# Performance work log

Measured on AMD Instinct MI355X. Metric: run time of the kernel, lower is better.

The kernel has to match this reference:

```python
import jax, jax.numpy as jnp
import numpy as np

EPS = 1e-5


def _layer(x, g, b, W_in, b_in, W_h, b_h, W_out, b_out):
    # x: [B, T, D]
    mu = jnp.mean(x, axis=-1, keepdims=True)
    var = jnp.mean(jnp.square(x - mu), axis=-1, keepdims=True)
    x_n = (x - mu) * jax.lax.rsqrt(var + EPS) * g + b
    # in_proj for all timesteps at once (same math as per-step linear)
    uv = jnp.einsum('btd,ed->bte', x_n, W_in) + b_in  # [B, T, 2D]
    d = x.shape[-1]
    u = jnp.transpose(uv[..., :d], (1, 0, 2))  # [T, B, D]
    v = jnp.transpose(uv[..., d:], (1, 0, 2))  # [T, B, D]

    def step(h, uv_t):
        u_t, v_t = uv_t
        gate = jax.nn.sigmoid(u_t)
        cand = jnp.tanh(v_t + h @ W_h.T + b_h)
        h_new = gate * cand + (1.0 - gate) * h
        y = h_new @ W_out.T + b_out
        return h_new, y

    h0 = jnp.zeros((x.shape[0], d), dtype=x.dtype)
    _, ys = jax.lax.scan(step, h0, (u, v))  # ys: [T, B, D]
    return x + jnp.transpose(ys, (1, 0, 2))


def setup_inputs() -> dict:
    key = jax.random.key(0)
    B, T, D, L = 8, 2048, 1024, 2
    ks = jax.random.split(key, 8)
    s = 1.0 / np.sqrt(D)
    return {
        'x': jax.random.normal(ks[0], (B, T, D), dtype=jnp.float32),
        'ln_g': jnp.ones((L, D), dtype=jnp.float32),
        'ln_b': jnp.zeros((L, D), dtype=jnp.float32),
        'W_in': jax.random.normal(ks[1], (L, 2 * D, D), dtype=jnp.float32) * s,
        'b_in': jnp.zeros((L, 2 * D), dtype=jnp.float32),
        'W_h': jax.random.normal(ks[2], (L, D, D), dtype=jnp.float32) * s,
        'b_h': jnp.zeros((L, D), dtype=jnp.float32),
        'W_out': jax.random.normal(ks[3], (L, D, D), dtype=jnp.float32) * s,
        'b_out': jnp.zeros((L, D), dtype=jnp.float32),
    }


def reference(x, ln_g, ln_b, W_in, b_in, W_h, b_h, W_out, b_out):
    out = x
    for l in range(W_in.shape[0]):  # small fixed n_layers loop
        out = _layer(out, ln_g[l], ln_b[l], W_in[l], b_in[l], W_h[l], b_h[l],
                     W_out[l], b_out[l])
    return out
```

## Files before the change

### kernel.cpp

```cpp
#include <hip/hip_runtime.h>
#include <stdint.h>
#include <stddef.h>

typedef __bf16 bf16;
typedef __bf16 bf16x8 __attribute__((ext_vector_type(8)));
typedef __bf16 bf16x4 __attribute__((ext_vector_type(4)));
typedef float  f32x4  __attribute__((ext_vector_type(4)));

#define B_ 8
#define T_ 2048
#define D_ 1024
#define L_ 2

#define AS1C(p) ((const __attribute__((address_space(1))) void*)(p))
#define AS3(p)  ((__attribute__((address_space(3))) void*)(p))


__global__ __launch_bounds__(256) void cvt_kernel(const float* __restrict__ in,
                                                  bf16* __restrict__ out, int n4) {
  int i = blockIdx.x * 256 + threadIdx.x;
  if (i >= n4) return;
  float4 v = ((const float4*)in)[i];
  bf16x4 o = { (bf16)v.x, (bf16)v.y, (bf16)v.z, (bf16)v.w };
  ((bf16x4*)out)[i] = o;
}

__global__ __launch_bounds__(256) void ln_kernel(const float* __restrict__ x,
                                                 const float* __restrict__ g,
                                                 const float* __restrict__ b,
                                                 bf16* __restrict__ xn) {
  const int row = blockIdx.x;
  const int tid = threadIdx.x;
  const float4 v = ((const float4*)(x + (size_t)row * D_))[tid];
  float s1 = v.x + v.y + v.z + v.w;
  float s2 = v.x * v.x + v.y * v.y + v.z * v.z + v.w * v.w;
#pragma unroll
  for (int off = 1; off < 64; off <<= 1) {
    s1 += __shfl_xor(s1, off);
    s2 += __shfl_xor(s2, off);
  }
  __shared__ float r1[4], r2[4];
  if ((tid & 63) == 0) { r1[tid >> 6] = s1; r2[tid >> 6] = s2; }
  __syncthreads();
  s1 = r1[0] + r1[1] + r1[2] + r1[3];
  s2 = r2[0] + r2[1] + r2[2] + r2[3];
  const float mu = s1 * (1.f / D_);
  const float var = s2 * (1.f / D_) - mu * mu;
  const float rs = rsqrtf(var + 1e-5f);
  const float4 gv = ((const float4*)g)[tid];
  const float4 bv = ((const float4*)b)[tid];
  bf16x4 o = { (bf16)((v.x - mu) * rs * gv.x + bv.x),
               (bf16)((v.y - mu) * rs * gv.y + bv.y),
               (bf16)((v.z - mu) * rs * gv.z + bv.z),
               (bf16)((v.w - mu) * rs * gv.w + bv.w) };
  ((bf16x4*)(xn + (size_t)row * D_))[tid] = o;
}

__global__ __launch_bounds__(256) void prep2_kernel(const float* __restrict__ Win2,
    const float* __restrict__ g2, const float* __restrict__ be2,
    const float* __restrict__ bin2, bf16* __restrict__ W2p,
    float* __restrict__ csum, float* __restrict__ cbias) {
  const int n = blockIdx.x;
  const int tid = threadIdx.x;
  const float4 w4 = ((const float4*)(Win2 + (size_t)n * 1024))[tid];
  const float4 g4 = ((const float4*)g2)[tid];
  const float4 b4 = ((const float4*)be2)[tid];
  bf16x4 o = { (bf16)(g4.x * w4.x), (bf16)(g4.y * w4.y),
               (bf16)(g4.z * w4.z), (bf16)(g4.w * w4.w) };
  ((bf16x4*)(W2p + (size_t)n * 1024))[tid] = o;
  float s = (float)o[0] + (float)o[1] + (float)o[2] + (float)o[3];
  float cbv = b4.x * w4.x + b4.y * w4.y + b4.z * w4.z + b4.w * w4.w;
#pragma unroll
  for (int off = 1; off < 64; off <<= 1) {
    s += __shfl_xor(s, off);
    cbv += __shfl_xor(cbv, off);
  }
  __shared__ float rs_[4], rc_[4];
  if ((tid & 63) == 0) { rs_[tid >> 6] = s; rc_[tid >> 6] = cbv; }
  __syncthreads();
  if (tid == 0) {
    csum[n] = rs_[0] + rs_[1] + rs_[2] + rs_[3];
    cbias[n] = rc_[0] + rc_[1] + rc_[2] + rc_[3] + bin2[n];
  }
}

__global__ __launch_bounds__(256) void gemm_uv(const bf16* __restrict__ A,
                                               const bf16* __restrict__ Bw,
                                               const float* __restrict__ bias,
                                               bf16* __restrict__ uvp,
                                               int M, int N, int K) {
  __shared__ bf16 As[128 * 32];
  __shared__ bf16 Bs[128 * 32];
  const int tid = threadIdx.x;
  const int lane = tid & 63;
  const int wave = tid >> 6;
  const int m0 = blockIdx.y * 128;
  const int n0 = blockIdx.x * 128;
  const int wm = (wave >> 1) * 64;
  const int wn = (wave & 1) * 64;
  f32x4 acc[4][4] = {};

  for (int kt = 0; kt < K; kt += 32) {
#pragma unroll
    for (int it = 0; it < 2; ++it) {
      const int gidx = it * 256 + tid;
      const int row = gidx >> 2;
      const int col = (gidx & 3) << 3;
      __builtin_amdgcn_global_load_lds(AS1C(A + (size_t)(m0 + row) * K + kt + col),
                                       AS3(&As[gidx * 8]), 16, 0, 0);
      __builtin_amdgcn_global_load_lds(AS1C(Bw + (size_t)(n0 + row) * K + kt + col),
                                       AS3(&Bs[gidx * 8]), 16, 0, 0);
    }
    __syncthreads();
    bf16x8 af[4], bfr[4];
#pragma unroll
    for (int i = 0; i < 4; ++i)
      af[i] = *(const bf16x8*)&As[(wm + i * 16 + (lane & 15)) * 32 + (lane >> 4) * 8];
#pragma unroll
    for (int j = 0; j < 4; ++j)
      bfr[j] = *(const bf16x8*)&Bs[(wn + j * 16 + (lane & 15)) * 32 + (lane >> 4) * 8];
#pragma unroll
    for (int i = 0; i < 4; ++i)
#pragma unroll
      for (int j = 0; j < 4; ++j)
        acc[i][j] = __builtin_amdgcn_mfma_f32_16x16x32_bf16(af[i], bfr[j], acc[i][j], 0, 0, 0);
    __syncthreads();
  }

  const int cr = (lane >> 4) * 4;
  const int cc = lane & 15;
#pragma unroll
  for (int i = 0; i < 4; ++i) {
#pragma unroll
    for (int j = 0; j < 4; ++j) {
      const int mb = m0 + wm + i * 16 + cr;
      const int n = n0 + wn + j * 16 + cc;
      const float bn = bias[n];
      const int p = n >> 10;
      const int nn2 = n & 1023;
#pragma unroll
      for (int r = 0; r < 4; ++r) {
        const int row = mb + r;
        const int b = row >> 11;
        const int t = row & (T_ - 1);
        uvp[(size_t)p * T_ * 8192 + (size_t)t * 8192 + nn2 * 8 + b] =
            (bf16)(acc[i][j][r] + bn);
      }
    }
  }
}

__global__ __launch_bounds__(256) void gemm_hfrag(const char* __restrict__ Hb,
                                                  const bf16* __restrict__ Bw,
                                                  const float* __restrict__ bias,
                                                  const char* __restrict__ residF,
                                                  float* __restrict__ C,
                                                  int M, int N, int K) {
  __shared__ bf16 As[128 * 32];
  __shared__ bf16 Bs[128 * 32];
  const int tid = threadIdx.x;
  const int lane = tid & 63;
  const int wave = tid >> 6;
  const int m0 = blockIdx.y * 128;
  const int n0 = blockIdx.x * 128;
  const int wm = (wave >> 1) * 64;
  const int wn = (wave & 1) * 64;
  f32x4 acc[4][4] = {};

  for (int kt = 0; kt < K; kt += 32) {
#pragma unroll
    for (int it = 0; it < 2; ++it) {
      const int g = it * 256 + tid;
      const int r = g >> 2;
      const int sub = g & 3;
      const int R = m0 + r;
      const int bb = R >> 11;
      const int tt = R & (T_ - 1);
      const char* src = Hb + (size_t)tt * 16384 + (size_t)(kt >> 5) * 512
                        + (sub * 8 + bb) * 16;
      __builtin_amdgcn_global_load_lds(AS1C(src), AS3(&As[g * 8]), 16, 0, 0);
      __builtin_amdgcn_global_load_lds(AS1C(Bw + (size_t)(n0 + r) * K + kt + (sub << 3)),
                                       AS3(&Bs[g * 8]), 16, 0, 0);
    }
    __syncthreads();
    bf16x8 af[4], bfr[4];
#pragma unroll
    for (int i = 0; i < 4; ++i)
      af[i] = *(const bf16x8*)&As[(wm + i * 16 + (lane & 15)) * 32 + (lane >> 4) * 8];
#pragma unroll
    for (int j = 0; j < 4; ++j)
      bfr[j] = *(const bf16x8*)&Bs[(wn + j * 16 + (lane & 15)) * 32 + (lane >> 4) * 8];
#pragma unroll
    for (int i = 0; i < 4; ++i)
#pragma unroll
      for (int j = 0; j < 4; ++j)
        acc[i][j] = __builtin_amdgcn_mfma_f32_16x16x32_bf16(af[i], bfr[j], acc[i][j], 0, 0, 0);
    __syncthreads();
  }

  const int cr = (lane >> 4) * 4;
  const int cc = lane & 15;
#pragma unroll
  for (int i = 0; i < 4; ++i) {
#pragma unroll
    for (int j = 0; j < 4; ++j) {
      const int mb = m0 + wm + i * 16 + cr;
      const int n = n0 + wn + j * 16 + cc;
      const float bn = bias[n];
      const int foffn = (n >> 5) * 512 + (((n & 31) >> 3) * 8) * 16 + (n & 7) * 2;
#pragma unroll
      for (int r = 0; r < 4; ++r) {
        const int row = mb + r;
        const int b = row >> 11;
        const int tt2 = row & (T_ - 1);
        const float resid =
            (float)*(const bf16*)(residF + (size_t)tt2 * 16384 + foffn + b * 16);
        C[(size_t)row * N + n] = acc[i][j][r] + bn + resid;
      }
    }
  }
}

__device__ __forceinline__ void load_wb(bf16x8 (&wB)[32], const bf16* Wrow) {
  const int half = ((threadIdx.x & 63) >> 4) << 3;
#pragma unroll
  for (int kk = 0; kk < 32; ++kk)
    wB[kk] = *(const bf16x8*)(Wrow + kk * 32 + half);
#pragma unroll
  for (int kk = 0; kk < 32; ++kk)
    asm volatile("" : "+a"(wB[kk]));
}

__device__ __forceinline__ f32x4 frag_matvec(const char* __restrict__ dF, int rdoff,
                                             const bf16x8 (&wB)[32]) {
  f32x4 a0 = {0.f, 0.f, 0.f, 0.f}, a1 = a0, a2 = a0, a3 = a0;
#pragma unroll
  for (int kk = 0; kk < 32; kk += 4) {
    bf16x8 f0 = *(const bf16x8*)(dF + kk * 512 + rdoff);
    bf16x8 f1 = *(const bf16x8*)(dF + (kk + 1) * 512 + rdoff);
    bf16x8 f2 = *(const bf16x8*)(dF + (kk + 2) * 512 + rdoff);
    bf16x8 f3 = *(const bf16x8*)(dF + (kk + 3) * 512 + rdoff);
    a0 = __builtin_amdgcn_mfma_f32_16x16x32_bf16(f0, wB[kk], a0, 0, 0, 0);
    a1 = __builtin_amdgcn_mfma_f32_16x16x32_bf16(f1, wB[kk + 1], a1, 0, 0, 0);
    a2 = __builtin_amdgcn_mfma_f32_16x16x32_bf16(f2, wB[kk + 2], a2, 0, 0, 0);
    a3 = __builtin_amdgcn_mfma_f32_16x16x32_bf16(f3, wB[kk + 3], a3, 0, 0, 0);
  }
  return (a0 + a1) + (a2 + a3);
}

__device__ __forceinline__ void poll8(const unsigned* base, unsigned tgt) {
  const int lane = threadIdx.x & 63;
  unsigned sv = tgt;
  if (lane < 8)
    sv = __hip_atomic_load(base + lane * 16, __ATOMIC_RELAXED, __HIP_MEMORY_SCOPE_AGENT);
  while (!__all((int)(sv >= tgt))) {
    __builtin_amdgcn_s_sleep(1);
    if (lane < 8)
      sv = __hip_atomic_load(base + lane * 16, __ATOMIC_RELAXED, __HIP_MEMORY_SCOPE_AGENT);
  }
  (void)__hip_atomic_load(base, __ATOMIC_ACQUIRE, __HIP_MEMORY_SCOPE_AGENT);
}

__device__ __forceinline__ void poll2s3(const unsigned* sync, int wg, unsigned tgt) {
  const int lane = threadIdx.x & 63;
  unsigned sv = tgt;
  if (lane < 2)
    sv = __hip_atomic_load(sync + 256 + ((lane ? 8 : 0) + wg) * 16,
                           __ATOMIC_RELAXED, __HIP_MEMORY_SCOPE_AGENT);
  while (!__all((int)(sv >= tgt))) {
    __builtin_amdgcn_s_sleep(1);
    if (lane < 2)
      sv = __hip_atomic_load(sync + 256 + ((lane ? 8 : 0) + wg) * 16,
                             __ATOMIC_RELAXED, __HIP_MEMORY_SCOPE_AGENT);
  }
  (void)__hip_atomic_load(sync + 256, __ATOMIC_ACQUIRE, __HIP_MEMORY_SCOPE_AGENT);
}

template <bool GATED>
__device__ __forceinline__ void scan_gang(int wg, const bf16* uvU, const bf16* uvV,
    const bf16* Wh, const float* bh, char* Hb, unsigned* sync, int ownBase,
    char (*hC)[16384], char (*tscr)[256]) {
  const int tid = threadIdx.x;
  const int lane = tid & 63;
  const int wv = tid >> 6;
  const int Wg = wg * 8 + wv;
  const int n0 = Wg * 16;
  const int c = lane & 15;

  bf16x8 wB[32];
  load_wb(wB, Wh + ((size_t)(n0 + c) << 10));

  const float bh_n = bh[n0 + c];
  const int b0 = (lane >> 4) * 4;
  const int rdoff = ((lane >> 4) * 8 + (lane & 7)) * 16;
  const int wregion = Wg * 256;

  float hs0 = 0.f, hs1 = 0.f, hs2 = 0.f, hs3 = 0.f;

  bf16x4 uq = {}, vq = {};
  if (GATED) poll2s3(sync, wg, 1u);
  if (lane < 32) {
    uq = *(const bf16x4*)(uvU + (n0 + c) * 8 + b0);
    vq = *(const bf16x4*)(uvV + (n0 + c) * 8 + b0);
  }

  for (int t = 0; t < T_; ++t) {
    f32x4 asum = {0.f, 0.f, 0.f, 0.f};
    if (t > 0) {
      poll8(sync + ownBase, (unsigned)t);
      __builtin_amdgcn_sched_barrier(0);
      const char* srcF = Hb + (size_t)(t - 1) * 16384;
      char* dstF = hC[t & 1];
      __builtin_amdgcn_global_load_lds(AS1C(srcF + tid * 16), AS3(dstF + tid * 16), 16, 0, 0);
      __builtin_amdgcn_global_load_lds(AS1C(srcF + (512 + tid) * 16),
                                       AS3(dstF + (512 + tid) * 16), 16, 0, 0);
      __syncthreads();
      asum = frag_matvec(dstF, rdoff, wB);
    }

    char* wscr = tscr[wv];
    if (lane < 32) {
#pragma unroll
      for (int r = 0; r < 4; ++r) {
        const float uu = (float)uq[r];
        const float vv = (float)vq[r];
        float& hh = (r == 0) ? hs0 : (r == 1) ? hs1 : (r == 2) ? hs2 : hs3;
        const float s = asum[r] + bh_n + vv;
        const float gg = __builtin_amdgcn_rcpf(1.f + __expf(-uu));
        const float e = __expf(2.f * s);
        const float cand = 1.f - 2.f * __builtin_amdgcn_rcpf(e + 1.f);
        hh = fmaf(gg, cand - hh, hh);
        *(bf16*)(wscr + (c >> 3) * 128 + (b0 + r) * 16 + (c & 7) * 2) = (bf16)hh;
      }
    }
    asm volatile("s_waitcnt lgkmcnt(0)" ::: "memory");
    __builtin_amdgcn_sched_barrier(0);
    if (lane < 32) {
      const unsigned long long pv = *(const unsigned long long*)(wscr + lane * 8);
      char* dst = Hb + (size_t)t * 16384 + wregion + lane * 8;
      __hip_atomic_store((unsigned long long*)dst, pv,
                         __ATOMIC_RELAXED, __HIP_MEMORY_SCOPE_AGENT);
    }
    __syncthreads();
    if (tid == 0)
      __hip_atomic_store(sync + ownBase + wg * 16, (unsigned)(t + 1),
                         __ATOMIC_RELEASE, __HIP_MEMORY_SCOPE_AGENT);
    __builtin_amdgcn_sched_barrier(0);
    if (t < T_ - 1) {
      if (GATED) poll2s3(sync, wg, (unsigned)(t + 2));
      if (lane < 32) {
        uq = *(const bf16x4*)(uvU + (size_t)(t + 1) * 8192 + (n0 + c) * 8 + b0);
        vq = *(const bf16x4*)(uvV + (size_t)(t + 1) * 8192 + (n0 + c) * 8 + b0);
      }
    }
  }
}

__device__ __forceinline__ void s2_gang(int wg, const char* H1, const bf16* Wout,
    const float* bout, const float* x, char* out1F, unsigned* sync,
    char (*hC)[16384], char (*tscr)[256]) {
  const int tid = threadIdx.x;
  const int lane = tid & 63;
  const int wv = tid >> 6;
  const int W2 = wg * 8 + wv;
  const int n0 = W2 * 16;
  const int c = lane & 15;

  bf16x8 wB[32];
  load_wb(wB, Wout + ((size_t)(n0 + c) << 10));

  const float bo = bout[n0 + c];
  const int b0 = (lane >> 4) * 4;
  const int rdoff = ((lane >> 4) * 8 + (lane & 7)) * 16;
  const int wregion = W2 * 256;

  f32x4 xq = {0.f, 0.f, 0.f, 0.f};
  if (lane < 32) {
#pragma unroll
    for (int r = 0; r < 4; ++r)
      xq[r] = x[((size_t)(b0 + r) * T_) * 1024 + n0 + c];
  }

  for (int t = 0; t < T_; ++t) {
    poll8(sync, (unsigned)(t + 1));
    __builtin_amdgcn_sched_barrier(0);
    const char* srcF = H1 + (size_t)t * 16384;
    char* dstF = hC[t & 1];
    __builtin_amdgcn_global_load_lds(AS1C(srcF + tid * 16), AS3(dstF + tid * 16), 16, 0, 0);
    __builtin_amdgcn_global_load_lds(AS1C(srcF + (512 + tid) * 16),
                                     AS3(dstF + (512 + tid) * 16), 16, 0, 0);
    __syncthreads();
    f32x4 asum = frag_matvec(dstF, rdoff, wB);

    char* wscr = tscr[wv];
    if (lane < 32) {
#pragma unroll
      for (int r = 0; r < 4; ++r) {
        const float o = xq[r] + asum[r] + bo;
        *(bf16*)(wscr + (c >> 3) * 128 + (b0 + r) * 16 + (c & 7) * 2) = (bf16)o;
      }
    }
    asm volatile("s_waitcnt lgkmcnt(0)" ::: "memory");
    __builtin_amdgcn_sched_barrier(0);
    if (lane < 32) {
      const unsigned long long pv = *(const unsigned long long*)(wscr + lane * 8);
      char* dst = out1F + (size_t)t * 16384 + wregion + lane * 8;
      __hip_atomic_store((unsigned long long*)dst, pv,
                         __ATOMIC_RELAXED, __HIP_MEMORY_SCOPE_AGENT);
    }
    __syncthreads();
    if (tid == 0)
      __hip_atomic_store(sync + 128 + wg * 16, (unsigned)(t + 1),
                         __ATOMIC_RELEASE, __HIP_MEMORY_SCOPE_AGENT);
    __builtin_amdgcn_sched_barrier(0);
    if (t < T_ - 1 && lane < 32) {
#pragma unroll
      for (int r = 0; r < 4; ++r)
        xq[r] = x[((size_t)(b0 + r) * T_ + (t + 1)) * 1024 + n0 + c];
    }
  }
}

__device__ __forceinline__ void s3_gang(int wg, const char* out1F, const bf16* W2p,
    const float* csum2, const float* cbias2, bf16* uv2, unsigned* sync,
    char (*hC)[16384], char (*tscr)[256], float* smu, float* srs) {
  const int tid = threadIdx.x;
  const int lane = tid & 63;
  const int wv = tid >> 6;
  const int W3 = wg * 8 + wv;
  const int c = lane & 15;
  const int n = W3 * 16 + c;

  bf16x8 wB[32];
  load_wb(wB, W2p + ((size_t)n << 10));

  const float cs = csum2[n];
  const float cb = cbias2[n];
  const int b0 = (lane >> 4) * 4;
  const int rdoff = ((lane >> 4) * 8 + (lane & 7)) * 16;
  char* outPlane = (char*)(uv2 + (size_t)(W3 >> 6) * T_ * 8192);
  const int nn = (W3 & 63) * 16;

  for (int t = 0; t < T_; ++t) {
    poll8(sync + 128, (unsigned)(t + 1));
    __builtin_amdgcn_sched_barrier(0);
    const char* srcF = out1F + (size_t)t * 16384;
    char* dstF = hC[t & 1];
    __builtin_amdgcn_global_load_lds(AS1C(srcF + tid * 16), AS3(dstF + tid * 16), 16, 0, 0);
    __builtin_amdgcn_global_load_lds(AS1C(srcF + (512 + tid) * 16),
                                     AS3(dstF + (512 + tid) * 16), 16, 0, 0);
    __syncthreads();
    {
      float s1 = 0.f, s2 = 0.f;
#pragma unroll
      for (int gi = 0; gi < 2; ++gi) {
        const int gr = lane * 2 + gi;
        bf16x8 v8 = *(const bf16x8*)(dstF + (gr >> 2) * 512 + ((gr & 3) * 8 + wv) * 16);
#pragma unroll
        for (int j = 0; j < 8; ++j) {
          const float f = (float)v8[j];
          s1 += f;
          s2 += f * f;
        }
      }
#pragma unroll
      for (int off = 1; off < 64; off <<= 1) {
        s1 += __shfl_xor(s1, off);
        s2 += __shfl_xor(s2, off);
      }
      if (lane == 0) {
        const float mu = s1 * (1.f / 1024.f);
        const float var = s2 * (1.f / 1024.f) - mu * mu;
        smu[wv] = mu;
        srs[wv] = rsqrtf(var + 1e-5f);
      }
    }
    __syncthreads();
    f32x4 asum = frag_matvec(dstF, rdoff, wB);

    char* wscr = tscr[wv];
    if (lane < 32) {
#pragma unroll
      for (int r = 0; r < 4; ++r) {
        const int b = b0 + r;
        const float val = srs[b] * (asum[r] - smu[b] * cs) + cb;
        *(bf16*)(wscr + c * 16 + b * 2) = (bf16)val;
      }
    }
    asm volatile("s_waitcnt lgkmcnt(0)" ::: "memory");
    __builtin_amdgcn_sched_barrier(0);
    if (lane < 32) {
      const unsigned long long pv = *(const unsigned long long*)(wscr + lane * 8);
      char* dst = outPlane + (size_t)t * 16384 + nn * 16 + lane * 8;
      __hip_atomic_store((unsigned long long*)dst, pv,
                         __ATOMIC_RELAXED, __HIP_MEMORY_SCOPE_AGENT);
    }
    __syncthreads();
    if (tid == 0)
      __hip_atomic_store(sync + 256 + wg * 16, (unsigned)(t + 1),
                         __ATOMIC_RELEASE, __HIP_MEMORY_SCOPE_AGENT);
    __builtin_amdgcn_sched_barrier(0);
  }
}

__global__ __launch_bounds__(512, 1) void mega_kernel(
    const bf16* __restrict__ uv1, const bf16* __restrict__ Wh,
    const float* __restrict__ bh, const bf16* __restrict__ Wout,
    const float* __restrict__ bout, const float* __restrict__ x,
    const bf16* __restrict__ W2p, const float* __restrict__ csum2,
    const float* __restrict__ cbias2, char* __restrict__ H1,
    char* __restrict__ out1F, bf16* __restrict__ uv2, char* __restrict__ H2,
    unsigned* __restrict__ sync) {
  __shared__ __align__(16) char hC[2][16384];
  __shared__ __align__(16) char tscr[8][256];
  __shared__ float smu[8], srs[8];
  const int bid = blockIdx.x;
  if (bid < 8) {
    scan_gang<false>(bid, uv1, uv1 + (size_t)T_ * 8192, Wh, bh, H1, sync, 0, hC, tscr);
  } else if (bid < 16) {
    s2_gang(bid - 8, H1, Wout, bout, x, out1F, sync, hC, tscr);
  } else if (bid < 32) {
    s3_gang(bid - 16, out1F, W2p, csum2, cbias2, uv2, sync, hC, tscr, smu, srs);
  } else {
    scan_gang<true>(bid - 32, uv2, uv2 + (size_t)T_ * 8192,
                    Wh + (size_t)D_ * D_, bh + D_, H2, sync, 512, hC, tscr);
  }
}

extern "C" void kernel_launch(void* const* d_in, const int* in_sizes, int n_in,
                              void* d_out, int out_size, void* d_ws, size_t ws_size,
                              hipStream_t stream) {
  const float* x     = (const float*)d_in[0];
  const float* ln_g  = (const float*)d_in[1];
  const float* ln_b  = (const float*)d_in[2];
  const float* W_in  = (const float*)d_in[3];
  const float* b_in  = (const float*)d_in[4];
  const float* W_h   = (const float*)d_in[5];
  const float* b_h   = (const float*)d_in[6];
  const float* W_out = (const float*)d_in[7];
  const float* b_out = (const float*)d_in[8];
  float* out = (float*)d_out;

  char* ws = (char*)d_ws;
  size_t off = 0;
  auto alloc = [&](size_t bytes) -> void* {
    void* p = ws + off;
    off = (off + bytes + 255) & ~(size_t)255;
    return p;
  };
  bf16* wInB   = (bf16*)alloc((size_t)L_ * 2 * D_ * D_ * 2);
  bf16* wHB    = (bf16*)alloc((size_t)L_ * D_ * D_ * 2);
  bf16* wOutB  = (bf16*)alloc((size_t)L_ * D_ * D_ * 2);
  bf16* W2p    = (bf16*)alloc((size_t)2 * D_ * D_ * 2);
  float* csum2 = (float*)alloc(2 * D_ * 4);
  float* cbias2= (float*)alloc(2 * D_ * 4);
  bf16* Xn     = (bf16*)alloc((size_t)B_ * T_ * D_ * 2);
  char* H2     = (char*)Xn;
  bf16* uvp1   = (bf16*)alloc((size_t)2 * T_ * 8192 * 2);
  char* H1     = (char*)alloc((size_t)T_ * 16384);
  char* out1F  = (char*)alloc((size_t)T_ * 16384);
  bf16* uvp2   = (bf16*)alloc((size_t)2 * T_ * 8192 * 2);
  unsigned* sync = (unsigned*)alloc(4096);
  (void)ws_size; (void)in_sizes; (void)n_in; (void)out_size;

  {
    int n4 = L_ * 2 * D_ * D_ / 4;
    cvt_kernel<<<(n4 + 255) / 256, 256, 0, stream>>>(W_in, wInB, n4);
    n4 = L_ * D_ * D_ / 4;
    cvt_kernel<<<(n4 + 255) / 256, 256, 0, stream>>>(W_h, wHB, n4);
    cvt_kernel<<<(n4 + 255) / 256, 256, 0, stream>>>(W_out, wOutB, n4);
  }
  prep2_kernel<<<2 * D_, 256, 0, stream>>>(W_in + (size_t)2 * D_ * D_,
                                           ln_g + D_, ln_b + D_, b_in + 2 * D_,
                                           W2p, csum2, cbias2);

  const int Mrows = B_ * T_;
  ln_kernel<<<Mrows, 256, 0, stream>>>(x, ln_g, ln_b, Xn);

  dim3 g1(2 * D_ / 128, Mrows / 128);
  gemm_uv<<<g1, 256, 0, stream>>>(Xn, wInB, b_in, uvp1, Mrows, 2 * D_, D_);

  hipMemsetAsync(sync, 0, 4096, stream);
  mega_kernel<<<40, 512, 0, stream>>>(uvp1, wHB, b_h, wOutB, b_out, x,
                                      W2p, csum2, cbias2, H1, out1F, uvp2, H2, sync);

  dim3 g2(D_ / 128, Mrows / 128);
  gemm_hfrag<<<g2, 256, 0, stream>>>(H2, wOutB + (size_t)D_ * D_, b_out + D_,
                                     out1F, out, Mrows, D_, D_);
}
```

Baseline: 11.37 ms.

## Prefetch next timestep into LDS and merge LayerNorm stats into one barrier

The s2 and s3 gangs now poll for step t+1 and issue its async global-to-LDS copy at the end of step t, so the copy overlaps the loop tail and the next barrier rather than sitting on the critical path. In s3, per-row partial sums are written to shared memory and combined after the matvec, which removes the separate barrier that came before the matvec. The scan gangs still depend on these stages each step, so the gain may be small. The double-buffered LDS reuse relies on the barrier ordering being correct.

```diff
diff --git a/kernel.cpp b/kernel.cpp
--- a/kernel.cpp
+++ b/kernel.cpp
@@ -276,6 +276,12 @@
   (void)__hip_atomic_load(sync + 256, __ATOMIC_ACQUIRE, __HIP_MEMORY_SCOPE_AGENT);
 }
 
+__device__ __forceinline__ void stage16k(const char* srcF, char* dstF, int tid) {
+  __builtin_amdgcn_global_load_lds(AS1C(srcF + tid * 16), AS3(dstF + tid * 16), 16, 0, 0);
+  __builtin_amdgcn_global_load_lds(AS1C(srcF + (512 + tid) * 16),
+                                   AS3(dstF + (512 + tid) * 16), 16, 0, 0);
+}
+
 template <bool GATED>
 __device__ __forceinline__ void scan_gang(int wg, const bf16* uvU, const bf16* uvV,
     const bf16* Wh, const float* bh, char* Hb, unsigned* sync, int ownBase,
@@ -309,13 +315,9 @@
     if (t > 0) {
       poll8(sync + ownBase, (unsigned)t);
       __builtin_amdgcn_sched_barrier(0);
-      const char* srcF = Hb + (size_t)(t - 1) * 16384;
-      char* dstF = hC[t & 1];
-      __builtin_amdgcn_global_load_lds(AS1C(srcF + tid * 16), AS3(dstF + tid * 16), 16, 0, 0);
-      __builtin_amdgcn_global_load_lds(AS1C(srcF + (512 + tid) * 16),
-                                       AS3(dstF + (512 + tid) * 16), 16, 0, 0);
+      stage16k(Hb + (size_t)(t - 1) * 16384, hC[t & 1], tid);
       __syncthreads();
-      asum = frag_matvec(dstF, rdoff, wB);
+      asum = frag_matvec(hC[t & 1], rdoff, wB);
     }
 
     char* wscr = tscr[wv];
@@ -381,16 +383,13 @@
       xq[r] = x[((size_t)(b0 + r) * T_) * 1024 + n0 + c];
   }
 
+  poll8(sync, 1u);
+  __builtin_amdgcn_sched_barrier(0);
+  stage16k(H1, hC[0], tid);
+
   for (int t = 0; t < T_; ++t) {
-    poll8(sync, (unsigned)(t + 1));
-    __builtin_amdgcn_sched_barrier(0);
-    const char* srcF = H1 + (size_t)t * 16384;
-    char* dstF = hC[t & 1];
-    __builtin_amdgcn_global_load_lds(AS1C(srcF + tid * 16), AS3(dstF + tid * 16), 16, 0, 0);
-    __builtin_amdgcn_global_load_lds(AS1C(srcF + (512 + tid) * 16),
-                                     AS3(dstF + (512 + tid) * 16), 16, 0, 0);
-    __syncthreads();
-    f32x4 asum = frag_matvec(dstF, rdoff, wB);
+    __syncthreads();
+    f32x4 asum = frag_matvec(hC[t & 1], rdoff, wB);
 
     char* wscr = tscr[wv];
     if (lane < 32) {
@@ -413,17 +412,22 @@
       __hip_atomic_store(sync + 128 + wg * 16, (unsigned)(t + 1),
                          __ATOMIC_RELEASE, __HIP_MEMORY_SCOPE_AGENT);
     __builtin_amdgcn_sched_barrier(0);
-    if (t < T_ - 1 && lane < 32) {
-#pragma unroll
-      for (int r = 0; r < 4; ++r)
-        xq[r] = x[((size_t)(b0 + r) * T_ + (t + 1)) * 1024 + n0 + c];
+    if (t + 1 < T_) {
+      poll8(sync, (unsigned)(t + 2));
+      __builtin_amdgcn_sched_barrier(0);
+      stage16k(H1 + (size_t)(t + 1) * 16384, hC[(t + 1) & 1], tid);
+      if (lane < 32) {
+#pragma unroll
+        for (int r = 0; r < 4; ++r)
+          xq[r] = x[((size_t)(b0 + r) * T_ + (t + 1)) * 1024 + n0 + c];
+      }
     }
   }
 }
 
 __device__ __forceinline__ void s3_gang(int wg, const char* out1F, const bf16* W2p,
     const float* csum2, const float* cbias2, bf16* uv2, unsigned* sync,
-    char (*hC)[16384], char (*tscr)[256], float* smu, float* srs) {
+    char (*hC)[16384], char (*tscr)[256], float* statp) {
   const int tid = threadIdx.x;
   const int lane = tid & 63;
   const int wv = tid >> 6;
@@ -440,50 +444,52 @@
   const int rdoff = ((lane >> 4) * 8 + (lane & 7)) * 16;
   char* outPlane = (char*)(uv2 + (size_t)(W3 >> 6) * T_ * 8192);
   const int nn = (W3 & 63) * 16;
+  const int sidx = wv * 128 + lane;
+
+  poll8(sync + 128, 1u);
+  __builtin_amdgcn_sched_barrier(0);
+  stage16k(out1F, hC[0], tid);
 
   for (int t = 0; t < T_; ++t) {
-    poll8(sync + 128, (unsigned)(t + 1));
-    __builtin_amdgcn_sched_barrier(0);
-    const char* srcF = out1F + (size_t)t * 16384;
-    char* dstF = hC[t & 1];
-    __builtin_amdgcn_global_load_lds(AS1C(srcF + tid * 16), AS3(dstF + tid * 16), 16, 0, 0);
-    __builtin_amdgcn_global_load_lds(AS1C(srcF + (512 + tid) * 16),
-                                     AS3(dstF + (512 + tid) * 16), 16, 0, 0);
-    __syncthreads();
+    __syncthreads();
+    const char* dstF = hC[t & 1];
     {
+      bf16x8 v0 = *(const bf16x8*)(dstF + sidx * 16);
+      bf16x8 v1 = *(const bf16x8*)(dstF + sidx * 16 + 1024);
       float s1 = 0.f, s2 = 0.f;
 #pragma unroll
-      for (int gi = 0; gi < 2; ++gi) {
-        const int gr = lane * 2 + gi;
-        bf16x8 v8 = *(const bf16x8*)(dstF + (gr >> 2) * 512 + ((gr & 3) * 8 + wv) * 16);
-#pragma unroll
-        for (int j = 0; j < 8; ++j) {
-          const float f = (float)v8[j];
-          s1 += f;
-          s2 += f * f;
-        }
-      }
-#pragma unroll
-      for (int off = 1; off < 64; off <<= 1) {
+      for (int j = 0; j < 8; ++j) {
+        const float f0 = (float)v0[j], f1 = (float)v1[j];
+        s1 += f0 + f1;
+        s2 += f0 * f0 + f1 * f1;
+      }
+#pragma unroll
+      for (int off = 8; off < 64; off <<= 1) {
         s1 += __shfl_xor(s1, off);
         s2 += __shfl_xor(s2, off);
       }
-      if (lane == 0) {
+      if (lane < 8) {
+        statp[(wv * 8 + lane) * 2] = s1;
+        statp[(wv * 8 + lane) * 2 + 1] = s2;
+      }
+    }
+    f32x4 asum = frag_matvec(dstF, rdoff, wB);
+    __syncthreads();
+    char* wscr = tscr[wv];
+    if (lane < 32) {
+#pragma unroll
+      for (int r = 0; r < 4; ++r) {
+        const int b = b0 + r;
+        float s1 = 0.f, s2 = 0.f;
+#pragma unroll
+        for (int w = 0; w < 8; ++w) {
+          s1 += statp[(w * 8 + b) * 2];
+          s2 += statp[(w * 8 + b) * 2 + 1];
+        }
         const float mu = s1 * (1.f / 1024.f);
         const float var = s2 * (1.f / 1024.f) - mu * mu;
-        smu[wv] = mu;
-        srs[wv] = rsqrtf(var + 1e-5f);
-      }
-    }
-    __syncthreads();
-    f32x4 asum = frag_matvec(dstF, rdoff, wB);
-
-    char* wscr = tscr[wv];
-    if (lane < 32) {
-#pragma unroll
-      for (int r = 0; r < 4; ++r) {
-        const int b = b0 + r;
-        const float val = srs[b] * (asum[r] - smu[b] * cs) + cb;
+        const float rs = rsqrtf(var + 1e-5f);
+        const float val = rs * (asum[r] - mu * cs) + cb;
         *(bf16*)(wscr + c * 16 + b * 2) = (bf16)val;
       }
     }
@@ -500,6 +506,11 @@
       __hip_atomic_store(sync + 256 + wg * 16, (unsigned)(t + 1),
                          __ATOMIC_RELEASE, __HIP_MEMORY_SCOPE_AGENT);
     __builtin_amdgcn_sched_barrier(0);
+    if (t + 1 < T_) {
+      poll8(sync + 128, (unsigned)(t + 2));
+      __builtin_amdgcn_sched_barrier(0);
+      stage16k(out1F + (size_t)(t + 1) * 16384, hC[(t + 1) & 1], tid);
+    }
   }
 }
 
@@ -513,14 +524,14 @@
     unsigned* __restrict__ sync) {
   __shared__ __align__(16) char hC[2][16384];
   __shared__ __align__(16) char tscr[8][256];
-  __shared__ float smu[8], srs[8];
+  __shared__ float statp[128];
   const int bid = blockIdx.x;
   if (bid < 8) {
     scan_gang<false>(bid, uv1, uv1 + (size_t)T_ * 8192, Wh, bh, H1, sync, 0, hC, tscr);
   } else if (bid < 16) {
     s2_gang(bid - 8, H1, Wout, bout, x, out1F, sync, hC, tscr);
   } else if (bid < 32) {
-    s3_gang(bid - 16, out1F, W2p, csum2, cbias2, uv2, sync, hC, tscr, smu, srs);
+    s3_gang(bid - 16, out1F, W2p, csum2, cbias2, uv2, sync, hC, tscr, statp);
   } else {
     scan_gang<true>(bid - 32, uv2, uv2 + (size_t)T_ * 8192,
                     Wh + (size_t)D_ * D_, bh + D_, H2, sync, 512, hC, tscr);
```

Result: faster. 11.13 ms (-2.1%).
